# Kernel optimization log

Hardware: AMD Instinct MI355X
Metric: run time of the kernel (lower is better)

## Reference

```python
import jax, jax.numpy as jnp
import numpy as np

N = 50000
E = 800000
NODE_CONT = 64
EDGE_CAT = 16
HID = 96
LAT = 64
NUM_LAYERS = 2
BN_EPS = 1e-5


def setup_inputs() -> dict:
    key = jax.random.key(0)
    ks = jax.random.split(key, 24)
    s = 0.05
    inp = {
        "x_cont": jax.random.normal(ks[0], (N, NODE_CONT), jnp.float32),
        "x_cat": jax.random.randint(ks[1], (N,), 0, 1),
        "edge_index": jax.random.randint(ks[2], (2, E), 0, N),
        "edge_attr_cat": jax.random.randint(ks[3], (E,), 0, EDGE_CAT),
        "edge_attr_cont": jax.random.normal(ks[4], (E, 1), jnp.float32),
        # parameters
        "w_node": jax.random.normal(ks[5], (HID, NODE_CONT), jnp.float32) * s,
        "b_node": jnp.zeros((HID,), jnp.float32),
        "edge_embed": jax.random.normal(ks[6], (EDGE_CAT, HID), jnp.float32) * s,
        "gcn_w": jax.random.normal(ks[7], (NUM_LAYERS, HID, HID), jnp.float32) * s,
        "gcn_b": jnp.zeros((NUM_LAYERS, HID), jnp.float32),
        "bn_gamma": jnp.ones((NUM_LAYERS, HID), jnp.float32),
        "bn_beta": jnp.zeros((NUM_LAYERS, HID), jnp.float32),
        "mlp_w1": jax.random.normal(ks[8], (NUM_LAYERS, HID, 2 * HID), jnp.float32) * s,
        "mlp_b1": jnp.zeros((NUM_LAYERS, HID), jnp.float32),
        "mlp_w2": jax.random.normal(ks[9], (NUM_LAYERS, HID, HID), jnp.float32) * s,
        "mlp_b2": jnp.zeros((NUM_LAYERS, HID), jnp.float32),
        "mu_w": jax.random.normal(ks[10], (LAT, HID), jnp.float32) * s,
        "mu_b": jnp.zeros((LAT,), jnp.float32),
        "lv_w": jax.random.normal(ks[11], (LAT, HID), jnp.float32) * s,
        "lv_b": jnp.zeros((LAT,), jnp.float32),
    }
    return inp


def _forward(x_cont, edge_index, edge_attr_cat,
             w_node, b_node, edge_embed,
             gcn_w, gcn_b, bn_gamma, bn_beta,
             mlp_w1, mlp_b1, mlp_w2, mlp_b2,
             mu_w, mu_b, lv_w, lv_b):
    n = x_cont.shape[0]
    # node embed (only continuous path active)
    h = x_cont @ w_node.T + b_node                      # [N, H]
    # edge embed (only categorical path active) -- memory-bound gather
    edge_h = edge_embed[edge_attr_cat]                  # [E, H]
    src, dst = edge_index[0], edge_index[1]
    # GCNConv: add self-loops, symmetric normalization
    loop = jnp.arange(n)
    src_f = jnp.concatenate([src, loop])
    dst_f = jnp.concatenate([dst, loop])
    deg = jax.ops.segment_sum(jnp.ones_like(dst_f, jnp.float32), dst_f, num_segments=n)
    dinv = jax.lax.rsqrt(deg)                           # deg >= 1 (self loops)
    norm = (dinv[src_f] * dinv[dst_f])[:, None]         # [E+N, 1]
    # edge_pooled: O(E) segment-mean replacing the O(N*E) python loop;
    # edge_h is constant across layers so compute it once.
    cnt = jax.ops.segment_sum(jnp.ones((edge_h.shape[0],), edge_h.dtype), dst, num_segments=n)
    pooled = jax.ops.segment_sum(edge_h, dst, num_segments=n) / jnp.maximum(cnt, 1.0)[:, None]
    for l in range(gcn_w.shape[0]):
        msg = (h @ gcn_w[l].T)[src_f] * norm            # gather + scale
        h_gnn = jax.ops.segment_sum(msg, dst_f, num_segments=n) + gcn_b[l]
        hc = jnp.concatenate([h_gnn, pooled], axis=-1)  # [N, 2H]
        h = jax.nn.relu(hc @ mlp_w1[l].T + mlp_b1[l]) @ mlp_w2[l].T + mlp_b2[l]
        # BatchNorm1d (training-mode batch stats, biased variance)
        mean = jnp.mean(h, axis=0)
        var = jnp.mean((h - mean) ** 2, axis=0)
        h = (h - mean) * jax.lax.rsqrt(var + BN_EPS) * bn_gamma[l] + bn_beta[l]
        h = jax.nn.relu(h)
        # dropout: eval mode (identity)
    mu = h @ mu_w.T + mu_b
    logvar = h @ lv_w.T + lv_b
    return mu, logvar


def reference(x_cont, x_cat, edge_index, edge_attr_cat, edge_attr_cont,
              w_node, b_node, edge_embed, gcn_w, gcn_b, bn_gamma, bn_beta,
              mlp_w1, mlp_b1, mlp_w2, mlp_b2, mu_w, mu_b, lv_w, lv_b):
    # x_cat and edge_attr_cont are unused: in_node_cat_dim=0, in_edge_cont_dim=0
    return _forward(x_cont, edge_index, edge_attr_cat,
                    w_node, b_node, edge_embed,
                    gcn_w, gcn_b, bn_gamma, bn_beta,
                    mlp_w1, mlp_b1, mlp_w2, mlp_b2,
                    mu_w, mu_b, lv_w, lv_b)
```

## Files before the change

kernel.cpp:

```cpp
#include <hip/hip_runtime.h>

#define N_NODES 50000
#define N_EDGES 800000
#define HID 96
#define NODE_CONT 64
#define LATD 64
#define EDGE_CATN 16
#define BN_EPS 1e-5f
#define CPAD 16
#define BCAP 48
#define NXCD 8
#define NODES_PER_XCD (N_NODES / NXCD)
#define BUILD_SUBS 128
#define EDGES_PER_SUB (N_EDGES / BUILD_SUBS)

typedef __attribute__((ext_vector_type(8))) short bf16x8;
typedef __attribute__((ext_vector_type(4))) float f32x4;

__device__ __forceinline__ unsigned short f2bf(float f) {
    union { float f; unsigned u; } c; c.f = f;
    unsigned r = (c.u + 0x7fffu + ((c.u >> 16) & 1u)) >> 16;
    return (unsigned short)r;
}
__device__ __forceinline__ float bf2f(unsigned short u) {
    union { unsigned u; float f; } c; c.u = ((unsigned)u) << 16;
    return c.f;
}

__global__ __launch_bounds__(256) void k_build(
    const int* __restrict__ ei, const int* __restrict__ ecat,
    int* __restrict__ cnt, int* __restrict__ csr)
{
    int xcd = blockIdx.x & (NXCD - 1);
    int sub = blockIdx.x >> 3;
    int lo = xcd * NODES_PER_XCD;
    int hi = lo + NODES_PER_XCD;
    int e1 = sub * EDGES_PER_SUB + EDGES_PER_SUB;
    for (int e = sub * EDGES_PER_SUB + threadIdx.x; e < e1; e += 256) {
        int dst = ei[N_EDGES + e];
        if (dst >= lo && dst < hi) {
            int r = atomicAdd(&cnt[dst * CPAD], 1);
            if (r < BCAP) csr[dst * BCAP + r] = (ei[e] << 4) | (ecat[e] & 15);
        }
    }
}

__global__ void k_dinv(const int* __restrict__ cnt, float* __restrict__ dinv) {
    int n = blockIdx.x * blockDim.x + threadIdx.x;
    if (n >= N_NODES) return;
    dinv[n] = rsqrtf((float)(cnt[n * CPAD] + 1));
}

template<int POOL>
__global__ __launch_bounds__(256) void k_aggregate(
    const int* __restrict__ csr, const int* __restrict__ cnt,
    const unsigned short* __restrict__ bt, const float* __restrict__ dinv,
    const float* __restrict__ gcn_b, unsigned short* __restrict__ bg,
    const float* __restrict__ eemb, unsigned short* __restrict__ bp)
{
    __shared__ float s_eemb[EDGE_CATN * HID];
    if constexpr (POOL) {
        for (int i = threadIdx.x; i < EDGE_CATN * HID; i += 256)
            s_eemb[i] = eemb[i];
        __syncthreads();
    }
    int node = blockIdx.x * 8 + (threadIdx.x >> 5);
    int lane = threadIdx.x & 31;
    if (node >= N_NODES) return;
    float dd = dinv[node];
    const unsigned short* tn = bt + (size_t)node * HID;
    float a0 = bf2f(tn[lane]);
    float a1 = bf2f(tn[lane + 32]);
    float a2 = bf2f(tn[lane + 64]);
    float p0 = 0.f, p1 = 0.f, p2 = 0.f;
    int deg = cnt[node * CPAD];
    if (deg > BCAP) deg = BCAP;
    int beg = node * BCAP, end = beg + deg;
    int p = beg;
    for (; p + 4 <= end; p += 4) {
        int e0 = csr[p], e1 = csr[p + 1], e2 = csr[p + 2], e3 = csr[p + 3];
        const unsigned short* r0 = bt + (size_t)(e0 >> 4) * HID;
        const unsigned short* r1 = bt + (size_t)(e1 >> 4) * HID;
        const unsigned short* r2 = bt + (size_t)(e2 >> 4) * HID;
        const unsigned short* r3 = bt + (size_t)(e3 >> 4) * HID;
        unsigned short v00 = r0[lane], v01 = r0[lane + 32], v02 = r0[lane + 64];
        unsigned short v10 = r1[lane], v11 = r1[lane + 32], v12 = r1[lane + 64];
        unsigned short v20 = r2[lane], v21 = r2[lane + 32], v22 = r2[lane + 64];
        unsigned short v30 = r3[lane], v31 = r3[lane + 32], v32 = r3[lane + 64];
        a0 += (bf2f(v00) + bf2f(v10)) + (bf2f(v20) + bf2f(v30));
        a1 += (bf2f(v01) + bf2f(v11)) + (bf2f(v21) + bf2f(v31));
        a2 += (bf2f(v02) + bf2f(v12)) + (bf2f(v22) + bf2f(v32));
        if constexpr (POOL) {
            const float* q0 = s_eemb + (e0 & 15) * HID;
            const float* q1 = s_eemb + (e1 & 15) * HID;
            const float* q2 = s_eemb + (e2 & 15) * HID;
            const float* q3 = s_eemb + (e3 & 15) * HID;
            p0 += (q0[lane] + q1[lane]) + (q2[lane] + q3[lane]);
            p1 += (q0[lane + 32] + q1[lane + 32]) + (q2[lane + 32] + q3[lane + 32]);
            p2 += (q0[lane + 64] + q1[lane + 64]) + (q2[lane + 64] + q3[lane + 64]);
        }
    }
    for (; p < end; ++p) {
        int e0 = csr[p];
        const unsigned short* r = bt + (size_t)(e0 >> 4) * HID;
        a0 += bf2f(r[lane]);
        a1 += bf2f(r[lane + 32]);
        a2 += bf2f(r[lane + 64]);
        if constexpr (POOL) {
            const float* q = s_eemb + (e0 & 15) * HID;
            p0 += q[lane]; p1 += q[lane + 32]; p2 += q[lane + 64];
        }
    }
    unsigned short* o = bg + (size_t)node * HID;
    o[lane]      = f2bf(a0 * dd + gcn_b[lane]);
    o[lane + 32] = f2bf(a1 * dd + gcn_b[lane + 32]);
    o[lane + 64] = f2bf(a2 * dd + gcn_b[lane + 64]);
    if constexpr (POOL) {
        float inv = 1.f / (float)(deg < 1 ? 1 : deg);
        unsigned short* ob = bp + (size_t)node * HID;
        ob[lane]      = f2bf(p0 * inv);
        ob[lane + 32] = f2bf(p1 * inv);
        ob[lane + 64] = f2bf(p2 * inv);
    }
}

#define OFF_WNODE 0
#define OFF_GCN   6144
#define OFF_W1    24576
#define OFF_W2    61440
#define OFF_MU    79872
#define OFF_LV    86016
#define W_TOTAL   92160

__global__ void k_wprep(const float* __restrict__ w_node, const float* __restrict__ gcn_w,
                        const float* __restrict__ w1, const float* __restrict__ w2,
                        const float* __restrict__ mu_w, const float* __restrict__ lv_w,
                        const float* __restrict__ b_node,
                        unsigned short* __restrict__ out, float* __restrict__ fused_b) {
    int i = blockIdx.x * blockDim.x + threadIdx.x;
    if (i < HID * NODE_CONT) {
        int j = i / NODE_CONT, k = i - j * NODE_CONT;
        float s = 0.f;
#pragma unroll 8
        for (int q = 0; q < HID; ++q) s += gcn_w[j * HID + q] * w_node[q * NODE_CONT + k];
        out[OFF_WNODE + i] = f2bf(s);
        if (k == 0) {
            float sb = 0.f;
#pragma unroll 8
            for (int q = 0; q < HID; ++q) sb += gcn_w[j * HID + q] * b_node[q];
            fused_b[j] = sb;
        }
    } else if (i < W_TOTAL) {
        float v;
        if (i < OFF_W1)       v = gcn_w[i - OFF_GCN];
        else if (i < OFF_W2)  v = w1[i - OFF_W1];
        else if (i < OFF_MU)  v = w2[i - OFF_W2];
        else if (i < OFF_LV)  v = mu_w[i - OFF_MU];
        else                  v = lv_w[i - OFF_LV];
        out[i] = f2bf(v);
    }
}

template<int NJT, int AF32>
__global__ __launch_bounds__(320) void k_gemm_bf(
    const void* __restrict__ A1v, int K1,
    const unsigned short* __restrict__ A2, int K2,
    const float* __restrict__ ss,
    const unsigned short* __restrict__ Wb,
    const float* __restrict__ bias, const float* __restrict__ bias2,
    const float* __restrict__ rowscale,
    unsigned short* __restrict__ Yb, float* __restrict__ Yf, float* __restrict__ Yf2,
    int act)
{
    const int K = K1 + K2;
    const int tile = blockIdx.x * 5 + (threadIdx.x >> 6);
    const int lane = threadIdx.x & 63;
    const int m = lane & 15;
    const int kg = lane >> 4;

    f32x4 acc[NJT];
#pragma unroll
    for (int jt = 0; jt < NJT; ++jt) acc[jt] = (f32x4){0.f, 0.f, 0.f, 0.f};

    const int arow = tile * 16 + m;

    for (int k0 = 0; k0 < K; k0 += 32) {
        int gk = k0 + kg * 8;
        bf16x8 a;
        if constexpr (AF32) {
            const float* apf = (const float*)A1v + (size_t)arow * K1 + gk;
            float4 x0 = *reinterpret_cast<const float4*>(apf);
            float4 x1 = *reinterpret_cast<const float4*>(apf + 4);
            a[0] = f2bf(x0.x); a[1] = f2bf(x0.y); a[2] = f2bf(x0.z); a[3] = f2bf(x0.w);
            a[4] = f2bf(x1.x); a[5] = f2bf(x1.y); a[6] = f2bf(x1.z); a[7] = f2bf(x1.w);
        } else {
            const unsigned short* A1 = (const unsigned short*)A1v;
            const unsigned short* ap = (gk < K1) ? A1 + (size_t)arow * K1 + gk
                                                 : A2 + (size_t)arow * K2 + (gk - K1);
            a = *reinterpret_cast<const bf16x8*>(ap);
            if (ss) {
#pragma unroll
                for (int i = 0; i < 8; ++i) {
                    float v = bf2f((unsigned short)a[i]);
                    v = fmaxf(v * ss[gk + i] + ss[96 + gk + i], 0.f);
                    a[i] = (short)f2bf(v);
                }
            }
        }
#pragma unroll
        for (int jt = 0; jt < NJT; ++jt) {
            const unsigned short* wp = Wb + (size_t)(jt * 16 + m) * K + gk;
            bf16x8 b = *reinterpret_cast<const bf16x8*>(wp);
            acc[jt] = __builtin_amdgcn_mfma_f32_16x16x32_bf16(a, b, acc[jt], 0, 0, 0);
        }
    }

    const int crow = tile * 16 + kg * 4;
    float rs[4] = {1.f, 1.f, 1.f, 1.f};
    if (rowscale) {
#pragma unroll
        for (int r = 0; r < 4; ++r) rs[r] = rowscale[crow + r];
    }
#pragma unroll
    for (int jt = 0; jt < NJT; ++jt) {
        int j = jt * 16 + m;
        float bv = 0.f;
        if (Yf2) bv = (jt < NJT / 2) ? bias[j] : bias2[j - (NJT / 2) * 16];
        else if (bias) bv = bias[j];
#pragma unroll
        for (int r = 0; r < 4; ++r) {
            float v = acc[jt][r] + bv;
            if (act) v = fmaxf(v, 0.f);
            v *= rs[r];
            int row = crow + r;
            if (Yf2) {
                if (jt < NJT / 2) Yf[(size_t)row * ((NJT / 2) * 16) + j] = v;
                else              Yf2[(size_t)row * ((NJT / 2) * 16) + (j - (NJT / 2) * 16)] = v;
            } else {
                Yb[(size_t)row * (NJT * 16) + j] = f2bf(v);
            }
        }
    }
}

__global__ __launch_bounds__(320) void k_mlp(
    const unsigned short* __restrict__ A1, const unsigned short* __restrict__ A2,
    const unsigned short* __restrict__ W1, const float* __restrict__ b1,
    const unsigned short* __restrict__ W2, const float* __restrict__ b2,
    unsigned short* __restrict__ bh, float* __restrict__ stats)
{
    __shared__ float s_stat[192];
    __shared__ unsigned short s_z1[5][16][104];
    for (int j = threadIdx.x; j < 192; j += 320) s_stat[j] = 0.f;
    const int wid = threadIdx.x >> 6;
    const int tile = blockIdx.x * 5 + wid;
    const int lane = threadIdx.x & 63;
    const int m = lane & 15;
    const int kg = lane >> 4;
    const int arow = tile * 16 + m;

    f32x4 acc[6];
#pragma unroll
    for (int jt = 0; jt < 6; ++jt) acc[jt] = (f32x4){0.f, 0.f, 0.f, 0.f};

    for (int k0 = 0; k0 < 192; k0 += 32) {
        int gk = k0 + kg * 8;
        const unsigned short* ap = (gk < 96) ? A1 + (size_t)arow * 96 + gk
                                             : A2 + (size_t)arow * 96 + (gk - 96);
        bf16x8 a = *reinterpret_cast<const bf16x8*>(ap);
#pragma unroll
        for (int jt = 0; jt < 6; ++jt) {
            bf16x8 b = *reinterpret_cast<const bf16x8*>(W1 + (size_t)(jt * 16 + m) * 192 + gk);
            acc[jt] = __builtin_amdgcn_mfma_f32_16x16x32_bf16(a, b, acc[jt], 0, 0, 0);
        }
    }
#pragma unroll
    for (int jt = 0; jt < 6; ++jt) {
        int j = jt * 16 + m;
        float bv = b1[j];
#pragma unroll
        for (int r = 0; r < 4; ++r)
            s_z1[wid][kg * 4 + r][j] = f2bf(fmaxf(acc[jt][r] + bv, 0.f));
    }
    __syncthreads();

    f32x4 acc2[6];
#pragma unroll
    for (int jt = 0; jt < 6; ++jt) acc2[jt] = (f32x4){0.f, 0.f, 0.f, 0.f};
    for (int k0 = 0; k0 < 96; k0 += 32) {
        int gk = k0 + kg * 8;
        bf16x8 a = *reinterpret_cast<const bf16x8*>(&s_z1[wid][m][gk]);
#pragma unroll
        for (int jt = 0; jt < 6; ++jt) {
            bf16x8 b = *reinterpret_cast<const bf16x8*>(W2 + (size_t)(jt * 16 + m) * 96 + gk);
            acc2[jt] = __builtin_amdgcn_mfma_f32_16x16x32_bf16(a, b, acc2[jt], 0, 0, 0);
        }
    }
    const int crow = tile * 16 + kg * 4;
#pragma unroll
    for (int jt = 0; jt < 6; ++jt) {
        int j = jt * 16 + m;
        float bv = b2[j];
        float lsum = 0.f, lsq = 0.f;
#pragma unroll
        for (int r = 0; r < 4; ++r) {
            float v = acc2[jt][r] + bv;
            lsum += v; lsq += v * v;
            bh[(size_t)(crow + r) * HID + j] = f2bf(v);
        }
        atomicAdd(&s_stat[j], lsum);
        atomicAdd(&s_stat[96 + j], lsq);
    }
    __syncthreads();
    for (int j = threadIdx.x; j < 192; j += 320) atomicAdd(&stats[j], s_stat[j]);
}

__global__ void k_bn_finalize(const float* __restrict__ stats,
                              const float* __restrict__ g, const float* __restrict__ b,
                              float* __restrict__ ss) {
    int j = threadIdx.x;
    if (j >= 96) return;
    float mean = stats[j] / (float)N_NODES;
    float var = stats[96 + j] / (float)N_NODES - mean * mean;
    float sc = g[j] * rsqrtf(var + BN_EPS);
    ss[j] = sc;
    ss[96 + j] = b[j] - mean * sc;
}

extern "C" void kernel_launch(void* const* d_in, const int* in_sizes, int n_in,
                              void* d_out, int out_size, void* d_ws, size_t ws_size,
                              hipStream_t stream) {
    const float* x_cont = (const float*)d_in[0];
    const int* edge_index = (const int*)d_in[2];
    const int* ecat = (const int*)d_in[3];
    const float* w_node = (const float*)d_in[5];
    const float* b_node = (const float*)d_in[6];
    const float* eemb = (const float*)d_in[7];
    const float* gcn_w = (const float*)d_in[8];
    const float* gcn_b = (const float*)d_in[9];
    const float* bn_g = (const float*)d_in[10];
    const float* bn_b = (const float*)d_in[11];
    const float* w1 = (const float*)d_in[12];
    const float* b1 = (const float*)d_in[13];
    const float* w2 = (const float*)d_in[14];
    const float* b2 = (const float*)d_in[15];
    const float* mu_w = (const float*)d_in[16];
    const float* mu_b = (const float*)d_in[17];
    const float* lv_w = (const float*)d_in[18];
    const float* lv_b = (const float*)d_in[19];
    float* out = (float*)d_out;

    char* base = (char*)d_ws;
    float* dinv    = (float*)base;                      base += (size_t)N_NODES * 4;
    float* statsA  = (float*)base;                      base += 2 * 192 * 4;
    float* ssbuf   = (float*)base;                      base += 2 * 192 * 4;
    float* fused_b = (float*)base;                      base += 128 * 4;
    int*   cnt     = (int*)base;                        base += (size_t)N_NODES * CPAD * 4;
    int*   csr     = (int*)base;                        base += (size_t)N_NODES * BCAP * 4;
    unsigned short* wbf = (unsigned short*)base;        base += (size_t)W_TOTAL * 2;
    unsigned short* bh  = (unsigned short*)base;        base += (size_t)N_NODES * HID * 2;
    unsigned short* bt  = (unsigned short*)base;        base += (size_t)N_NODES * HID * 2;
    unsigned short* bg  = (unsigned short*)base;        base += (size_t)N_NODES * HID * 2;
    unsigned short* bp  = (unsigned short*)base;        base += (size_t)N_NODES * HID * 2;

    hipMemsetAsync(cnt, 0, (size_t)N_NODES * CPAD * sizeof(int), stream);
    hipMemsetAsync(statsA, 0, 2 * 192 * sizeof(float), stream);

    k_wprep<<<(W_TOTAL + 255) / 256, 256, 0, stream>>>(w_node, gcn_w, w1, w2, mu_w, lv_w,
                                                       b_node, wbf, fused_b);
    k_build<<<NXCD * BUILD_SUBS, 256, 0, stream>>>(edge_index, ecat, cnt, csr);
    k_dinv<<<(N_NODES + 255) / 256, 256, 0, stream>>>(cnt, dinv);

    const int GG = N_NODES / 16 / 5;

    for (int l = 0; l < 2; ++l) {
        if (l == 0)
            k_gemm_bf<6, 1><<<GG, 320, 0, stream>>>(x_cont, NODE_CONT, nullptr, 0, nullptr,
                                                    wbf + OFF_WNODE, fused_b, nullptr, dinv,
                                                    bt, nullptr, nullptr, 0);
        else
            k_gemm_bf<6, 0><<<GG, 320, 0, stream>>>(bh, HID, nullptr, 0, ssbuf,
                                                    wbf + OFF_GCN + l * HID * HID,
                                                    nullptr, nullptr, dinv,
                                                    bt, nullptr, nullptr, 0);
        if (l == 0)
            k_aggregate<1><<<N_NODES / 8, 256, 0, stream>>>(
                csr, cnt, bt, dinv, gcn_b + l * HID, bg, eemb, bp);
        else
            k_aggregate<0><<<N_NODES / 8, 256, 0, stream>>>(
                csr, cnt, bt, dinv, gcn_b + l * HID, bg, eemb, bp);
        k_mlp<<<GG, 320, 0, stream>>>(bg, bp,
                                      wbf + OFF_W1 + l * HID * 2 * HID, b1 + l * HID,
                                      wbf + OFF_W2 + l * HID * HID, b2 + l * HID,
                                      bh, statsA + l * 192);
        k_bn_finalize<<<1, 128, 0, stream>>>(statsA + l * 192, bn_g + l * HID, bn_b + l * HID,
                                             ssbuf + l * 192);
    }

    k_gemm_bf<8, 0><<<GG, 320, 0, stream>>>(bh, HID, nullptr, 0, ssbuf + 192,
                                            wbf + OFF_MU, mu_b, lv_b, nullptr,
                                            nullptr, out, out + (size_t)N_NODES * LATD, 0);
}
```

Baseline: 246.4 us.

## Simplify CSR build, templatize GEMM K, replace BN atomics with partial reduction

The XCD-partitioned CSR build is replaced with one thread per edge doing a global atomic on the destination count. The GEMM kernel now takes K1/K2 as template parameters, so the K loops can be fully unrolled, and the MLP K loops are also unrolled. The per-block atomic accumulation of BatchNorm statistics is replaced by per-block partial writes, reduced by a new 96-block kernel, which also removes a memset. The simpler build reads each edge once instead of eight times, but may lose the L2 locality the XCD partitioning aimed for.

```diff
diff --git a/kernel.cpp b/kernel.cpp
--- a/kernel.cpp
+++ b/kernel.cpp
@@ -9,10 +9,7 @@
 #define BN_EPS 1e-5f
 #define CPAD 16
 #define BCAP 48
-#define NXCD 8
-#define NODES_PER_XCD (N_NODES / NXCD)
-#define BUILD_SUBS 128
-#define EDGES_PER_SUB (N_EDGES / BUILD_SUBS)
+#define MLP_BLOCKS 625
 
 typedef __attribute__((ext_vector_type(8))) short bf16x8;
 typedef __attribute__((ext_vector_type(4))) float f32x4;
@@ -27,22 +24,13 @@
     return c.f;
 }
 
-__global__ __launch_bounds__(256) void k_build(
-    const int* __restrict__ ei, const int* __restrict__ ecat,
-    int* __restrict__ cnt, int* __restrict__ csr)
-{
-    int xcd = blockIdx.x & (NXCD - 1);
-    int sub = blockIdx.x >> 3;
-    int lo = xcd * NODES_PER_XCD;
-    int hi = lo + NODES_PER_XCD;
-    int e1 = sub * EDGES_PER_SUB + EDGES_PER_SUB;
-    for (int e = sub * EDGES_PER_SUB + threadIdx.x; e < e1; e += 256) {
-        int dst = ei[N_EDGES + e];
-        if (dst >= lo && dst < hi) {
-            int r = atomicAdd(&cnt[dst * CPAD], 1);
-            if (r < BCAP) csr[dst * BCAP + r] = (ei[e] << 4) | (ecat[e] & 15);
-        }
-    }
+__global__ void k_build(const int* __restrict__ ei, const int* __restrict__ ecat,
+                        int* __restrict__ cnt, int* __restrict__ csr) {
+    int e = blockIdx.x * blockDim.x + threadIdx.x;
+    if (e >= N_EDGES) return;
+    int dst = ei[N_EDGES + e];
+    int r = atomicAdd(&cnt[dst * CPAD], 1);
+    if (r < BCAP) csr[dst * BCAP + r] = (ei[e] << 4) | (ecat[e] & 15);
 }
 
 __global__ void k_dinv(const int* __restrict__ cnt, float* __restrict__ dinv) {
@@ -161,10 +149,10 @@
     }
 }
 
-template<int NJT, int AF32>
+template<int NJT, int AF32, int K1, int K2>
 __global__ __launch_bounds__(320) void k_gemm_bf(
-    const void* __restrict__ A1v, int K1,
-    const unsigned short* __restrict__ A2, int K2,
+    const void* __restrict__ A1v,
+    const unsigned short* __restrict__ A2,
     const float* __restrict__ ss,
     const unsigned short* __restrict__ Wb,
     const float* __restrict__ bias, const float* __restrict__ bias2,
@@ -172,7 +160,7 @@
     unsigned short* __restrict__ Yb, float* __restrict__ Yf, float* __restrict__ Yf2,
     int act)
 {
-    const int K = K1 + K2;
+    constexpr int K = K1 + K2;
     const int tile = blockIdx.x * 5 + (threadIdx.x >> 6);
     const int lane = threadIdx.x & 63;
     const int m = lane & 15;
@@ -184,6 +172,7 @@
 
     const int arow = tile * 16 + m;
 
+#pragma unroll
     for (int k0 = 0; k0 < K; k0 += 32) {
         int gk = k0 + kg * 8;
         bf16x8 a;
@@ -247,7 +236,7 @@
     const unsigned short* __restrict__ A1, const unsigned short* __restrict__ A2,
     const unsigned short* __restrict__ W1, const float* __restrict__ b1,
     const unsigned short* __restrict__ W2, const float* __restrict__ b2,
-    unsigned short* __restrict__ bh, float* __restrict__ stats)
+    unsigned short* __restrict__ bh, float* __restrict__ partials)
 {
     __shared__ float s_stat[192];
     __shared__ unsigned short s_z1[5][16][104];
@@ -263,6 +252,7 @@
 #pragma unroll
     for (int jt = 0; jt < 6; ++jt) acc[jt] = (f32x4){0.f, 0.f, 0.f, 0.f};
 
+#pragma unroll
     for (int k0 = 0; k0 < 192; k0 += 32) {
         int gk = k0 + kg * 8;
         const unsigned short* ap = (gk < 96) ? A1 + (size_t)arow * 96 + gk
@@ -287,6 +277,7 @@
     f32x4 acc2[6];
 #pragma unroll
     for (int jt = 0; jt < 6; ++jt) acc2[jt] = (f32x4){0.f, 0.f, 0.f, 0.f};
+#pragma unroll
     for (int k0 = 0; k0 < 96; k0 += 32) {
         int gk = k0 + kg * 8;
         bf16x8 a = *reinterpret_cast<const bf16x8*>(&s_z1[wid][m][gk]);
@@ -312,19 +303,34 @@
         atomicAdd(&s_stat[96 + j], lsq);
     }
     __syncthreads();
-    for (int j = threadIdx.x; j < 192; j += 320) atomicAdd(&stats[j], s_stat[j]);
-}
-
-__global__ void k_bn_finalize(const float* __restrict__ stats,
-                              const float* __restrict__ g, const float* __restrict__ b,
-                              float* __restrict__ ss) {
-    int j = threadIdx.x;
-    if (j >= 96) return;
-    float mean = stats[j] / (float)N_NODES;
-    float var = stats[96 + j] / (float)N_NODES - mean * mean;
-    float sc = g[j] * rsqrtf(var + BN_EPS);
-    ss[j] = sc;
-    ss[96 + j] = b[j] - mean * sc;
+    float* prow = partials + (size_t)blockIdx.x * 192;
+    for (int j = threadIdx.x; j < 192; j += 320) prow[j] = s_stat[j];
+}
+
+__global__ __launch_bounds__(64) void k_bn_reduce(
+    const float* __restrict__ partials,
+    const float* __restrict__ g, const float* __restrict__ b,
+    float* __restrict__ ss)
+{
+    int j = blockIdx.x;
+    int t = threadIdx.x;
+    float s = 0.f, s2 = 0.f;
+    for (int i = t; i < MLP_BLOCKS; i += 64) {
+        s  += partials[(size_t)i * 192 + j];
+        s2 += partials[(size_t)i * 192 + 96 + j];
+    }
+#pragma unroll
+    for (int off = 32; off > 0; off >>= 1) {
+        s  += __shfl_down(s, off, 64);
+        s2 += __shfl_down(s2, off, 64);
+    }
+    if (t == 0) {
+        float mean = s / (float)N_NODES;
+        float var = s2 / (float)N_NODES - mean * mean;
+        float sc = g[j] * rsqrtf(var + BN_EPS);
+        ss[j] = sc;
+        ss[96 + j] = b[j] - mean * sc;
+    }
 }
 
 extern "C" void kernel_launch(void* const* d_in, const int* in_sizes, int n_in,
@@ -351,12 +357,12 @@
     float* out = (float*)d_out;
 
     char* base = (char*)d_ws;
-    float* dinv    = (float*)base;                      base += (size_t)N_NODES * 4;
-    float* statsA  = (float*)base;                      base += 2 * 192 * 4;
-    float* ssbuf   = (float*)base;                      base += 2 * 192 * 4;
-    float* fused_b = (float*)base;                      base += 128 * 4;
-    int*   cnt     = (int*)base;                        base += (size_t)N_NODES * CPAD * 4;
-    int*   csr     = (int*)base;                        base += (size_t)N_NODES * BCAP * 4;
+    float* dinv     = (float*)base;                     base += (size_t)N_NODES * 4;
+    float* partials = (float*)base;                     base += (size_t)MLP_BLOCKS * 192 * 4;
+    float* ssbuf    = (float*)base;                     base += 2 * 192 * 4;
+    float* fused_b  = (float*)base;                     base += 128 * 4;
+    int*   cnt      = (int*)base;                       base += (size_t)N_NODES * CPAD * 4;
+    int*   csr      = (int*)base;                       base += (size_t)N_NODES * BCAP * 4;
     unsigned short* wbf = (unsigned short*)base;        base += (size_t)W_TOTAL * 2;
     unsigned short* bh  = (unsigned short*)base;        base += (size_t)N_NODES * HID * 2;
     unsigned short* bt  = (unsigned short*)base;        base += (size_t)N_NODES * HID * 2;
@@ -364,25 +370,23 @@
     unsigned short* bp  = (unsigned short*)base;        base += (size_t)N_NODES * HID * 2;
 
     hipMemsetAsync(cnt, 0, (size_t)N_NODES * CPAD * sizeof(int), stream);
-    hipMemsetAsync(statsA, 0, 2 * 192 * sizeof(float), stream);
 
     k_wprep<<<(W_TOTAL + 255) / 256, 256, 0, stream>>>(w_node, gcn_w, w1, w2, mu_w, lv_w,
                                                        b_node, wbf, fused_b);
-    k_build<<<NXCD * BUILD_SUBS, 256, 0, stream>>>(edge_index, ecat, cnt, csr);
+    k_build<<<(N_EDGES + 255) / 256, 256, 0, stream>>>(edge_index, ecat, cnt, csr);
     k_dinv<<<(N_NODES + 255) / 256, 256, 0, stream>>>(cnt, dinv);
 
     const int GG = N_NODES / 16 / 5;
 
     for (int l = 0; l < 2; ++l) {
         if (l == 0)
-            k_gemm_bf<6, 1><<<GG, 320, 0, stream>>>(x_cont, NODE_CONT, nullptr, 0, nullptr,
-                                                    wbf + OFF_WNODE, fused_b, nullptr, dinv,
-                                                    bt, nullptr, nullptr, 0);
+            k_gemm_bf<6, 1, NODE_CONT, 0><<<GG, 320, 0, stream>>>(
+                x_cont, nullptr, nullptr, wbf + OFF_WNODE, fused_b, nullptr, dinv,
+                bt, nullptr, nullptr, 0);
         else
-            k_gemm_bf<6, 0><<<GG, 320, 0, stream>>>(bh, HID, nullptr, 0, ssbuf,
-                                                    wbf + OFF_GCN + l * HID * HID,
-                                                    nullptr, nullptr, dinv,
-                                                    bt, nullptr, nullptr, 0);
+            k_gemm_bf<6, 0, HID, 0><<<GG, 320, 0, stream>>>(
+                bh, nullptr, ssbuf, wbf + OFF_GCN + l * HID * HID,
+                nullptr, nullptr, dinv, bt, nullptr, nullptr, 0);
         if (l == 0)
             k_aggregate<1><<<N_NODES / 8, 256, 0, stream>>>(
                 csr, cnt, bt, dinv, gcn_b + l * HID, bg, eemb, bp);
@@ -392,12 +396,12 @@
         k_mlp<<<GG, 320, 0, stream>>>(bg, bp,
                                       wbf + OFF_W1 + l * HID * 2 * HID, b1 + l * HID,
                                       wbf + OFF_W2 + l * HID * HID, b2 + l * HID,
-                                      bh, statsA + l * 192);
-        k_bn_finalize<<<1, 128, 0, stream>>>(statsA + l * 192, bn_g + l * HID, bn_b + l * HID,
-                                             ssbuf + l * 192);
-    }
-
-    k_gemm_bf<8, 0><<<GG, 320, 0, stream>>>(bh, HID, nullptr, 0, ssbuf + 192,
-                                            wbf + OFF_MU, mu_b, lv_b, nullptr,
-                                            nullptr, out, out + (size_t)N_NODES * LATD, 0);
-}
+                                      bh, partials);
+        k_bn_reduce<<<96, 64, 0, stream>>>(partials, bn_g + l * HID, bn_b + l * HID,
+                                           ssbuf + l * 192);
+    }
+
+    k_gemm_bf<8, 0, HID, 0><<<GG, 320, 0, stream>>>(
+        bh, nullptr, ssbuf + 192, wbf + OFF_MU, mu_b, lv_b, nullptr,
+        nullptr, out, out + (size_t)N_NODES * LATD, 0);
+}
```

New measurement: 251.6 us. +2.1%, slower.
